# Performance work log

Measured on AMD Instinct MI355X. Metric: run time of the kernel, lower is better.

The kernel has to match this reference:

```python
import jax, jax.numpy as jnp
import numpy as np

B, S, HID = 1, 2048, 2048
NUM_HEADS, NUM_KV_HEADS, HEAD_DIM = 16, 4, 128
ROPE_THETA = 10000.0
EPS = 1e-6


def setup_inputs() -> dict:
    key = jax.random.key(0)
    ks = jax.random.split(key, 9)
    s = 0.02
    return {
        "hidden_states": jax.random.normal(ks[0], (B, S, HID), jnp.float32),
        "mu_prev": jax.random.normal(ks[1], (B, S, HID), jnp.float32),
        "wq": jax.random.normal(ks[2], (NUM_HEADS * HEAD_DIM, HID), jnp.float32) * s,
        "wk": jax.random.normal(ks[3], (NUM_KV_HEADS * HEAD_DIM, HID), jnp.float32) * s,
        "wv": jax.random.normal(ks[4], (NUM_KV_HEADS * HEAD_DIM, HID), jnp.float32) * s,
        "wo": jax.random.normal(ks[5], (HID, NUM_HEADS * HEAD_DIM), jnp.float32) * s,
        "wmq": jax.random.normal(ks[6], (NUM_HEADS * HEAD_DIM, HID), jnp.float32) * (s * 0.1),
        "wmk": jax.random.normal(ks[7], (NUM_KV_HEADS * HEAD_DIM, HID), jnp.float32) * (s * 0.1),
        "wmv": jax.random.normal(ks[8], (NUM_KV_HEADS * HEAD_DIM, HID), jnp.float32) * (s * 0.1),
        "q_norm_w": jnp.ones((HEAD_DIM,), jnp.float32),
        "k_norm_w": jnp.ones((HEAD_DIM,), jnp.float32),
    }


def _rmsnorm(x, w):
    var = jnp.mean(jnp.square(x), axis=-1, keepdims=True)
    return x * jax.lax.rsqrt(var + EPS) * w


def _rope_cos_sin(seq_len, dtype):
    inv_freq = 1.0 / (ROPE_THETA ** (jnp.arange(0, HEAD_DIM, 2, dtype=jnp.float32) / HEAD_DIM))
    freqs = jnp.arange(seq_len, dtype=jnp.float32)[:, None] * inv_freq[None, :]  # [S, D/2]
    emb = jnp.concatenate([freqs, freqs], axis=-1)  # [S, D]
    return jnp.cos(emb).astype(dtype), jnp.sin(emb).astype(dtype)


def _rotate_half(x):
    x1, x2 = jnp.split(x, 2, axis=-1)
    return jnp.concatenate([-x2, x1], axis=-1)


def reference(hidden_states, mu_prev, wq, wk, wv, wo, wmq, wmk, wmv, q_norm_w, k_norm_w):
    b, s, _ = hidden_states.shape
    # Fused mu-guided QKV projections (cat(x, mu) @ cat(W, Wm)^T == x@W^T + mu@Wm^T)
    q = hidden_states @ wq.T + mu_prev @ wmq.T  # [B,S,H*D]
    k = hidden_states @ wk.T + mu_prev @ wmk.T  # [B,S,KV*D]
    v = hidden_states @ wv.T + mu_prev @ wmv.T
    q = q.reshape(b, s, NUM_HEADS, HEAD_DIM).transpose(0, 2, 1, 3)      # [B,H,S,D]
    k = k.reshape(b, s, NUM_KV_HEADS, HEAD_DIM).transpose(0, 2, 1, 3)   # [B,KV,S,D]
    v = v.reshape(b, s, NUM_KV_HEADS, HEAD_DIM).transpose(0, 2, 1, 3)
    # per-head QK RMSNorm
    q = _rmsnorm(q, q_norm_w)
    k = _rmsnorm(k, k_norm_w)
    # RoPE
    cos, sin = _rope_cos_sin(s, q.dtype)
    q = q * cos + _rotate_half(q) * sin
    k = k * cos + _rotate_half(k) * sin
    # GQA attention without materializing repeated K/V: group query heads
    g = NUM_HEADS // NUM_KV_HEADS
    qg = q.reshape(b, NUM_KV_HEADS, g, s, HEAD_DIM)
    scale = 1.0 / jnp.sqrt(jnp.asarray(HEAD_DIM, q.dtype))
    scores = jnp.einsum('bkgqd,bkld->bkgql', qg, k) * scale  # [B,KV,G,S,S]
    causal = jnp.tril(jnp.ones((s, s), bool))
    scores = jnp.where(causal, scores, jnp.asarray(-jnp.inf, scores.dtype))
    probs = jax.nn.softmax(scores.astype(jnp.float32), axis=-1).astype(q.dtype)
    out = jnp.einsum('bkgql,bkld->bkgqd', probs, v)  # [B,KV,G,S,D]
    out = out.reshape(b, NUM_HEADS, s, HEAD_DIM).transpose(0, 2, 1, 3).reshape(b, s, NUM_HEADS * HEAD_DIM)
    return out @ wo.T
```

## Files before the change

kernel.cpp:

```cpp
#include <hip/hip_runtime.h>
#include <math.h>

#define SEQ 2048
#define HID_DIM 2048
#define NH 16
#define NKV 4
#define HD 128
#define QS 3072

typedef float  f4v  __attribute__((ext_vector_type(4)));
typedef __bf16 bf8v __attribute__((ext_vector_type(8)));
typedef __bf16 bf4v __attribute__((ext_vector_type(4)));
typedef __bf16 bf2v __attribute__((ext_vector_type(2)));

typedef __attribute__((address_space(1))) const void* gvp;
typedef __attribute__((address_space(3))) void*       svp;

__device__ __forceinline__ void gld16(const void* g, void* lds_wave_base) {
    __builtin_amdgcn_global_load_lds((gvp)g, (svp)lds_wave_base, 16, 0, 0);
}

__device__ __forceinline__ void wgb() {
    asm volatile("" ::: "memory");
    __builtin_amdgcn_s_barrier();
    asm volatile("" ::: "memory");
}
#define LGKM0 do { asm volatile("s_waitcnt lgkmcnt(0)" ::: "memory"); \
                   __builtin_amdgcn_sched_barrier(0); } while (0)
#define VMC(n) asm volatile("s_waitcnt vmcnt(" #n ")" ::: "memory")

__global__ __launch_bounds__(256)
void cvt_cat2(__bf16* __restrict__ dst, const float* __restrict__ s0,
              const float* __restrict__ s1, int rows, int kq)
{
    int i = blockIdx.x * 256 + threadIdx.x;
    if (i >= rows * kq * 2) return;
    int row = i / (2 * kq), c = i - row * 2 * kq;
    const float* s = (c < kq) ? s0 + ((size_t)row * kq + c) * 4
                              : s1 + ((size_t)row * kq + (c - kq)) * 4;
    float4 v = *reinterpret_cast<const float4*>(s);
    *reinterpret_cast<bf4v*>(dst + ((size_t)row * 2 * kq + c) * 4) =
        bf4v{ (__bf16)v.x, (__bf16)v.y, (__bf16)v.z, (__bf16)v.w };
}

__global__ __launch_bounds__(256)
void cvt(__bf16* __restrict__ dst, const float* __restrict__ src, int n4)
{
    int i = blockIdx.x * 256 + threadIdx.x;
    if (i >= n4) return;
    float4 v = *reinterpret_cast<const float4*>(src + (size_t)i * 4);
    *reinterpret_cast<bf4v*>(dst + (size_t)i * 4) =
        bf4v{ (__bf16)v.x, (__bf16)v.y, (__bf16)v.z, (__bf16)v.w };
}

__device__ __forceinline__ void stage_half(
    const __bf16* __restrict__ g, int ldk, int row0, int ktile, int half,
    char* buf, int w, int sr, int sc)
{
#pragma unroll
    for (int j = 0; j < 2; ++j) {
        int sid = w * 2 + j;
        int rb = half * 8 + (sid >> 1), cb = sid & 1;
        gld16(g + (size_t)(row0 + rb * 16 + sr) * ldk + ktile * 64 + cb * 32 + sc,
              buf + (rb * 2 + cb) * 1024);
    }
}

#define LOAD_A(BUF, MTB) \
    _Pragma("unroll") for (int mt = 0; mt < 4; ++mt) \
    _Pragma("unroll") for (int ks = 0; ks < 2; ++ks) \
        a[mt][ks] = *(const bf8v*)((BUF) + (((wm * 8 + (MTB) + mt) * 2 + ks) << 10) + frag_off);
#define LOAD_B(BUF, NTB, BR) \
    _Pragma("unroll") for (int nt = 0; nt < 2; ++nt) \
    _Pragma("unroll") for (int ks = 0; ks < 2; ++ks) \
        BR[nt][ks] = *(const bf8v*)((BUF) + (((wn * 4 + (NTB) + nt) * 2 + ks) << 10) + frag_off);
#define MFMA_Q(MTB, NTB, BR) \
    __builtin_amdgcn_s_setprio(1); \
    _Pragma("unroll") for (int mt = 0; mt < 4; ++mt) \
    _Pragma("unroll") for (int nt = 0; nt < 2; ++nt) \
    _Pragma("unroll") for (int ks = 0; ks < 2; ++ks) \
        acc[(MTB) + mt][(NTB) + nt] = __builtin_amdgcn_mfma_f32_16x16x32_bf16( \
            a[mt][ks], BR[nt][ks], acc[(MTB) + mt][(NTB) + nt], 0, 0, 0); \
    __builtin_amdgcn_s_setprio(0);

__global__ __launch_bounds__(512, 2)
void gemm_nt_8p(const __bf16* __restrict__ A, const __bf16* __restrict__ B,
                __bf16* __restrict__ P, int M, int N, int K, int KS)
{
    __shared__ __align__(1024) char lds[131072];
    char* A0 = lds;
    char* A1 = lds + 32768;
    char* B0 = lds + 65536;
    char* B1 = lds + 98304;

    const int tid = threadIdx.x, lane = tid & 63, w = tid >> 6;
    const int wm = w >> 2, wn = w & 3;
    const int mm = lane & 15, quad = lane >> 4;
    const int m0 = blockIdx.y * 256, n0 = blockIdx.x * 256;
    const int kt0 = (blockIdx.z * KS) >> 6;
    const int T = KS >> 6;

    const int g2 = lane ^ ((lane >> 4) & 3);
    const int sr = g2 >> 2, sc = (g2 & 3) * 8;
    const int gl = mm * 4 + quad;
    const int frag_off = (gl ^ ((gl >> 4) & 3)) << 4;

    f4v acc[8][4] = {};
    bf8v a[4][2], b01[2][2], b23[2][2];

    stage_half(A, K, m0, kt0,     0, A0, w, sr, sc);
    stage_half(A, K, m0, kt0,     1, A0, w, sr, sc);
    stage_half(B, K, n0, kt0,     0, B0, w, sr, sc);
    stage_half(B, K, n0, kt0,     1, B0, w, sr, sc);
    stage_half(A, K, m0, kt0 + 1, 0, A1, w, sr, sc);
    stage_half(A, K, m0, kt0 + 1, 1, A1, w, sr, sc);
    stage_half(B, K, n0, kt0 + 1, 0, B1, w, sr, sc);
    stage_half(B, K, n0, kt0 + 1, 1, B1, w, sr, sc);
    VMC(8);
    wgb();

    for (int t = 0; t < T; t += 2) {
        const bool more = (t + 2) < T;
        const int t2 = kt0 + t + 2, t3 = kt0 + t + 3;
        LOAD_A(A0, 0)
        LOAD_B(B0, 0, b01)
        wgb(); LGKM0;
        MFMA_Q(0, 0, b01)
        wgb();
        LOAD_B(B0, 2, b23)
        wgb(); LGKM0;
        MFMA_Q(0, 2, b23)
        wgb();
        LOAD_A(A0, 4)
        if (more) stage_half(B, K, n0, t2, 0, B0, w, sr, sc);
        wgb(); LGKM0;
        MFMA_Q(4, 2, b23)
        wgb();
        if (more) {
            stage_half(B, K, n0, t2, 1, B0, w, sr, sc);
            stage_half(A, K, m0, t2, 0, A0, w, sr, sc);
        }
        MFMA_Q(4, 0, b01)
        if (more) { VMC(6); } else { VMC(0); }
        wgb();
        LOAD_A(A1, 0)
        LOAD_B(B1, 0, b01)
        if (more) stage_half(A, K, m0, t2, 1, A0, w, sr, sc);
        wgb(); LGKM0;
        MFMA_Q(0, 0, b01)
        wgb();
        LOAD_B(B1, 2, b23)
        wgb(); LGKM0;
        MFMA_Q(0, 2, b23)
        wgb();
        LOAD_A(A1, 4)
        if (more) stage_half(B, K, n0, t3, 0, B1, w, sr, sc);
        wgb(); LGKM0;
        MFMA_Q(4, 2, b23)
        wgb();
        if (more) {
            stage_half(B, K, n0, t3, 1, B1, w, sr, sc);
            stage_half(A, K, m0, t3, 0, A1, w, sr, sc);
            stage_half(A, K, m0, t3, 1, A1, w, sr, sc);
        }
        MFMA_Q(4, 0, b01)
        if (more) { VMC(8); }
        wgb();
    }

    __bf16* Pz = P + (size_t)blockIdx.z * M * N;
#pragma unroll
    for (int mt = 0; mt < 8; ++mt)
#pragma unroll
        for (int nt = 0; nt < 4; ++nt)
#pragma unroll
            for (int r = 0; r < 4; ++r)
                Pz[(size_t)(m0 + wm * 128 + mt * 16 + quad * 4 + r) * N
                   + n0 + wn * 64 + nt * 16 + mm] = (__bf16)acc[mt][nt][r];
}

__global__ __launch_bounds__(256)
void add4(const __bf16* __restrict__ P, float* __restrict__ out, int n4)
{
    int i = blockIdx.x * 256 + threadIdx.x;
    if (i >= n4) return;
    float4 s = {0.f, 0.f, 0.f, 0.f};
#pragma unroll
    for (int z = 0; z < 4; ++z) {
        bf4v v = *reinterpret_cast<const bf4v*>(P + (size_t)z * n4 * 4 + (size_t)i * 4);
        s.x += (float)v[0]; s.y += (float)v[1]; s.z += (float)v[2]; s.w += (float)v[3];
    }
    *reinterpret_cast<float4*>(out + (size_t)i * 4) = s;
}

__global__ __launch_bounds__(64)
void norm_rope(__bf16* __restrict__ qkv ,
               const __bf16* __restrict__ p1,
               const float* __restrict__ qw, const float* __restrict__ kw)
{
    const int s = blockIdx.x, hh = blockIdx.y, l = threadIdx.x;
    const float* wn; float scale; int off;
    if (hh < NH) { off = hh * HD;               wn = qw; scale = 0.08838834764831845f; }
    else         { off = 2048 + (hh - NH) * HD; wn = kw; scale = 1.0f; }
    __bf16* p = qkv + (size_t)s * QS + off;
    const __bf16* q1 = p1 + (size_t)s * QS + off;
    float x0 = (float)p[l]      + (float)q1[l];
    float x1 = (float)p[l + 64] + (float)q1[l + 64];
    float ss = x0 * x0 + x1 * x1;
#pragma unroll
    for (int o = 32; o; o >>= 1) ss += __shfl_xor(ss, o);
    float inv = rsqrtf(ss * (1.0f / 128.0f) + 1e-6f);
    x0 *= inv * wn[l];
    x1 *= inv * wn[l + 64];
    float invf = exp2f(-(float)l * (13.287712379549449f / 64.0f));
    float ang  = (float)s * invf;
    float c, sn;
    sincosf(ang, &sn, &c);
    p[l]      = (__bf16)((x0 * c - x1 * sn) * scale);
    p[l + 64] = (__bf16)((x1 * c + x0 * sn) * scale);
}

__global__ __launch_bounds__(256)
void pack_k(const __bf16* __restrict__ qkv, __bf16* __restrict__ Kt)
{
    const int kt = blockIdx.x, kh = blockIdx.y, t = threadIdx.x;
    char* tile = (char*)Kt + ((size_t)(kh * 32 + kt)) * 16384;
    const __bf16* src = qkv + 2048 + kh * HD;
#pragma unroll
    for (int i = 0; i < 4; ++i) {
        int cid = t * 4 + i;
        int key = cid >> 4, pc = cid & 15;
        int c = pc ^ (key & 15);
        bf8v v = *reinterpret_cast<const bf8v*>(src + (size_t)(kt * 64 + key) * QS + c * 8);
        *reinterpret_cast<bf8v*>(tile + cid * 16) = v;
    }
}

__global__ __launch_bounds__(256)
void pack_v(const __bf16* __restrict__ qkv0, const __bf16* __restrict__ qkv1,
            __bf16* __restrict__ Vt)
{
    const int kt = blockIdx.x, kh = blockIdx.y, t = threadIdx.x;
    char* tile = (char*)Vt + ((size_t)(kh * 32 + kt)) * 16384;
    const __bf16* s0 = qkv0 + 2560 + kh * HD;
    const __bf16* s1 = qkv1 + 2560 + kh * HD;
#pragma unroll
    for (int i = 0; i < 4; ++i) {
        int cid = t * 4 + i;
        int d = cid >> 3, kcp = cid & 7;
        int kc = kcp ^ (d & 7);
        size_t base = (size_t)(kt * 64 + kc * 8) * QS + d;
        __bf16 tmp[8];
#pragma unroll
        for (int j = 0; j < 8; ++j)
            tmp[j] = (__bf16)((float)s0[base + (size_t)j * QS] +
                              (float)s1[base + (size_t)j * QS]);
        *reinterpret_cast<bf8v*>(tile + cid * 16) = *reinterpret_cast<bf8v*>(tmp);
    }
}

__global__ __launch_bounds__(256)
void attn_split(const __bf16* __restrict__ qkv,
                const __bf16* __restrict__ Kt, const __bf16* __restrict__ Vt,
                __bf16* __restrict__ Op, float* __restrict__ Lp)
{
    __shared__ char Ks[16384];
    __shared__ char Vs[16384];
    __shared__ char Ps[4][2048];

    const int c = blockIdx.x, qt = 31 - blockIdx.y, h = blockIdx.z;
    if (c * 8 > qt) return;
    const int kend = min(qt, c * 8 + 7);
    const int tid = threadIdx.x, lane = tid & 63, w = tid >> 6;
    const int mm = lane & 15, quad = lane >> 4;
    const int kh = h >> 2;

    bf8v aq[4];
    const __bf16* qbase = qkv + (size_t)(qt * 64 + w * 16 + mm) * QS + h * HD;
#pragma unroll
    for (int ks = 0; ks < 4; ++ks)
        aq[ks] = *reinterpret_cast<const bf8v*>(qbase + ks * 32 + quad * 8);

    float lp[4] = {};
    f4v oacc[8] = {};

    for (int kt = c * 8; kt <= kend; ++kt) {
        __syncthreads();
        const char* ktile = (const char*)Kt + ((size_t)(kh * 32 + kt)) * 16384;
        const char* vtile = (const char*)Vt + ((size_t)(kh * 32 + kt)) * 16384;
#pragma unroll
        for (int j = 0; j < 4; ++j) {
            int chunk = w * 4 + j;
            gld16(ktile + chunk * 1024 + lane * 16, Ks + chunk * 1024);
            gld16(vtile + chunk * 1024 + lane * 16, Vs + chunk * 1024);
        }
        __syncthreads();

        f4v s[4] = {};
#pragma unroll
        for (int ks = 0; ks < 4; ++ks)
#pragma unroll
            for (int c16 = 0; c16 < 4; ++c16) {
                bf8v b = *reinterpret_cast<const bf8v*>(
                    Ks + (c16 * 16 + mm) * 256 + (((ks * 4 + quad) ^ mm) << 4));
                s[c16] = __builtin_amdgcn_mfma_f32_16x16x32_bf16(aq[ks], b, s[c16], 0, 0, 0);
            }
        if (kt == qt) {
#pragma unroll
            for (int c16 = 0; c16 < 4; ++c16)
#pragma unroll
                for (int r = 0; r < 4; ++r)
                    if (c16 * 16 + mm > w * 16 + quad * 4 + r)
                        s[c16][r] = -__builtin_inff();
        }
        float pr[4][4];
#pragma unroll
        for (int c16 = 0; c16 < 4; ++c16)
#pragma unroll
            for (int r = 0; r < 4; ++r) {
                pr[c16][r] = __expf(s[c16][r]);
                lp[r] += pr[c16][r];
            }
#pragma unroll
        for (int c16 = 0; c16 < 4; ++c16)
#pragma unroll
            for (int r = 0; r < 4; ++r) {
                float mine  = pr[c16][r];
                float other = __shfl_xor(mine, 1);
                if ((mm & 1) == 0) {
                    int roww = quad * 4 + r;
                    int cc   = c16 * 2 + (mm >> 3);
                    *reinterpret_cast<bf2v*>(
                        &Ps[w][roww * 128 + ((cc ^ (roww & 7)) << 4) + (mm & 7) * 2]) =
                        bf2v{ (__bf16)mine, (__bf16)other };
                }
            }
        bf8v pa[2];
#pragma unroll
        for (int kb = 0; kb < 2; ++kb)
            pa[kb] = *reinterpret_cast<const bf8v*>(
                &Ps[w][mm * 128 + (((kb * 4 + quad) ^ (mm & 7)) << 4)]);
#pragma unroll
        for (int nb = 0; nb < 8; ++nb) {
            int d = nb * 16 + mm;
#pragma unroll
            for (int kb = 0; kb < 2; ++kb) {
                bf8v bv = *reinterpret_cast<const bf8v*>(
                    Vs + d * 128 + (((kb * 4 + quad) ^ (d & 7)) << 4));
                oacc[nb] = __builtin_amdgcn_mfma_f32_16x16x32_bf16(pa[kb], bv, oacc[nb], 0, 0, 0);
            }
        }
    }
#pragma unroll
    for (int off = 1; off < 16; off <<= 1)
#pragma unroll
        for (int r = 0; r < 4; ++r) lp[r] += __shfl_xor(lp[r], off);
#pragma unroll
    for (int r = 0; r < 4; ++r) {
        int row = qt * 64 + w * 16 + quad * 4 + r;
        size_t obase = ((size_t)(c * 16 + h) * SEQ + row) * HD;
#pragma unroll
        for (int nb = 0; nb < 8; ++nb)
            Op[obase + nb * 16 + mm] = (__bf16)oacc[nb][r];
        if (mm == 0)
            Lp[(size_t)(c * 16 + h) * SEQ + row] = lp[r];
    }
}

__global__ __launch_bounds__(64)
void combine(const __bf16* __restrict__ Op, const float* __restrict__ Lp,
             __bf16* __restrict__ ab)
{
    const int row = blockIdx.x, h = blockIdx.y, l = threadIdx.x;
    const int nch = (row >> 9) + 1;
    float L = 0.f, a0 = 0.f, a1 = 0.f;
    for (int c = 0; c < nch; ++c) {
        L += Lp[(size_t)(c * 16 + h) * SEQ + row];
        bf2v p = *reinterpret_cast<const bf2v*>(
            Op + ((size_t)(c * 16 + h) * SEQ + row) * HD + 2 * l);
        a0 += (float)p[0];
        a1 += (float)p[1];
    }
    float inv = 1.f / L;
    *reinterpret_cast<bf2v*>(ab + (size_t)row * (NH * HD) + h * HD + 2 * l) =
        bf2v{ (__bf16)(a0 * inv), (__bf16)(a1 * inv) };
}

extern "C" void kernel_launch(void* const* d_in, const int* in_sizes, int n_in,
                              void* d_out, int out_size, void* d_ws, size_t ws_size,
                              hipStream_t stream)
{
    const float* hs  = (const float*)d_in[0];
    const float* mu  = (const float*)d_in[1];
    const float* wq  = (const float*)d_in[2];
    const float* wk  = (const float*)d_in[3];
    const float* wv  = (const float*)d_in[4];
    const float* wo  = (const float*)d_in[5];
    const float* wmq = (const float*)d_in[6];
    const float* wmk = (const float*)d_in[7];
    const float* wmv = (const float*)d_in[8];
    const float* qw  = (const float*)d_in[9];
    const float* kw  = (const float*)d_in[10];
    float* out = (float*)d_out;

    char* ws = (char*)d_ws;
    __bf16* Wcat = (__bf16*)(ws + 0);
    __bf16* Acat = (__bf16*)(ws + 25165824);
    __bf16* Wo   = (__bf16*)(ws + 41943040);
    __bf16* qkvp = (__bf16*)(ws + 50331648);
    __bf16* ab   = (__bf16*)(ws + 75497472);
    __bf16* Ktl  = (__bf16*)(ws + 0);
    __bf16* Vtl  = (__bf16*)(ws + 2097152);
    __bf16* Opart= (__bf16*)(ws + 4194304);
    float*  Lpart= (float*) (ws + 37748736);
    __bf16* outp = (__bf16*)(ws + 0);

    cvt_cat2<<<dim3((2048 * 1024 + 255) / 256), 256, 0, stream>>>(Acat, hs, mu, 2048, 512);
    cvt_cat2<<<dim3((2048 * 1024 + 255) / 256), 256, 0, stream>>>(Wcat, wq, wmq, 2048, 512);
    cvt_cat2<<<dim3((512 * 1024 + 255) / 256), 256, 0, stream>>>(Wcat + (size_t)2048 * 4096, wk, wmk, 512, 512);
    cvt_cat2<<<dim3((512 * 1024 + 255) / 256), 256, 0, stream>>>(Wcat + (size_t)2560 * 4096, wv, wmv, 512, 512);
    cvt<<<dim3((1024 * 1024 + 255) / 256), 256, 0, stream>>>(Wo, wo, 1024 * 1024);

    gemm_nt_8p<<<dim3(QS / 256, SEQ / 256, 2), 512, 0, stream>>>(Acat, Wcat, qkvp, SEQ, QS, 2 * HID_DIM, HID_DIM);
    norm_rope<<<dim3(SEQ, NH + NKV), dim3(64), 0, stream>>>(qkvp, qkvp + (size_t)SEQ * QS, qw, kw);
    pack_k<<<dim3(32, NKV), 256, 0, stream>>>(qkvp, Ktl);
    pack_v<<<dim3(32, NKV), 256, 0, stream>>>(qkvp, qkvp + (size_t)SEQ * QS, Vtl);
    attn_split<<<dim3(4, 32, NH), 256, 0, stream>>>(qkvp, Ktl, Vtl, Opart, Lpart);
    combine<<<dim3(SEQ, NH), 64, 0, stream>>>(Opart, Lpart, ab);
    gemm_nt_8p<<<dim3(HID_DIM / 256, SEQ / 256, 4), 512, 0, stream>>>(ab, Wo, outp, SEQ, HID_DIM, NH * HD, 512);
    add4<<<dim3((1024 * 1024 + 255) / 256), 256, 0, stream>>>(outp, out, 1024 * 1024);
}
```

Baseline: 359.7 us.

## Software-pipeline LDS fragment loads across MFMA quadrants in GEMM kernel

Restructures the GEMM main loop so the LDS fragment reads for the next quadrant are issued before the current quadrant's MFMAs. Explicit lgkmcnt waits are removed, and A and B register fragments are double-buffered (aLo/aHi, b01e/b01o). The LDS XOR swizzle is dropped in favour of a plain linear fragment layout. Global staging is regrouped into whole-tile loads with a full vmcnt(0) wait, and a peeled epilogue handles the last two k-tiles. The aim is to overlap LDS latency with MFMA work, at the cost of more registers, possible LDS bank conflicts without the swizzle, and stricter global-load waits.

```diff
diff --git a/kernel.cpp b/kernel.cpp
--- a/kernel.cpp
+++ b/kernel.cpp
@@ -25,8 +25,6 @@
     __builtin_amdgcn_s_barrier();
     asm volatile("" ::: "memory");
 }
-#define LGKM0 do { asm volatile("s_waitcnt lgkmcnt(0)" ::: "memory"); \
-                   __builtin_amdgcn_sched_barrier(0); } while (0)
 #define VMC(n) asm volatile("s_waitcnt vmcnt(" #n ")" ::: "memory")
 
 __global__ __launch_bounds__(256)
@@ -65,26 +63,33 @@
               buf + (rb * 2 + cb) * 1024);
     }
 }
-
-#define LOAD_A(BUF, MTB) \
+__device__ __forceinline__ void stage_tile(
+    const __bf16* __restrict__ g, int ldk, int row0, int ktile,
+    char* buf, int w, int sr, int sc)
+{
+    stage_half(g, ldk, row0, ktile, 0, buf, w, sr, sc);
+    stage_half(g, ldk, row0, ktile, 1, buf, w, sr, sc);
+}
+
+#define LOAD_AF(DST, BUF, MTB) \
     _Pragma("unroll") for (int mt = 0; mt < 4; ++mt) \
     _Pragma("unroll") for (int ks = 0; ks < 2; ++ks) \
-        a[mt][ks] = *(const bf8v*)((BUF) + (((wm * 8 + (MTB) + mt) * 2 + ks) << 10) + frag_off);
-#define LOAD_B(BUF, NTB, BR) \
+        DST[mt][ks] = *(const bf8v*)((BUF) + (((wm * 8 + (MTB) + mt) * 2 + ks) << 10) + frag_off);
+#define LOAD_BF(DST, BUF, NTB) \
     _Pragma("unroll") for (int nt = 0; nt < 2; ++nt) \
     _Pragma("unroll") for (int ks = 0; ks < 2; ++ks) \
-        BR[nt][ks] = *(const bf8v*)((BUF) + (((wn * 4 + (NTB) + nt) * 2 + ks) << 10) + frag_off);
-#define MFMA_Q(MTB, NTB, BR) \
+        DST[nt][ks] = *(const bf8v*)((BUF) + (((wn * 4 + (NTB) + nt) * 2 + ks) << 10) + frag_off);
+#define MFMA_Q(MTB, NTB, AR, BR) \
     __builtin_amdgcn_s_setprio(1); \
     _Pragma("unroll") for (int mt = 0; mt < 4; ++mt) \
     _Pragma("unroll") for (int nt = 0; nt < 2; ++nt) \
     _Pragma("unroll") for (int ks = 0; ks < 2; ++ks) \
         acc[(MTB) + mt][(NTB) + nt] = __builtin_amdgcn_mfma_f32_16x16x32_bf16( \
-            a[mt][ks], BR[nt][ks], acc[(MTB) + mt][(NTB) + nt], 0, 0, 0); \
+            AR[mt][ks], BR[nt][ks], acc[(MTB) + mt][(NTB) + nt], 0, 0, 0); \
     __builtin_amdgcn_s_setprio(0);
 
 __global__ __launch_bounds__(512, 2)
-void gemm_nt_8p(const __bf16* __restrict__ A, const __bf16* __restrict__ B,
+void gemm_nt_pl(const __bf16* __restrict__ A, const __bf16* __restrict__ B,
                 __bf16* __restrict__ P, int M, int N, int K, int KS)
 {
     __shared__ __align__(1024) char lds[131072];
@@ -100,73 +105,76 @@
     const int kt0 = (blockIdx.z * KS) >> 6;
     const int T = KS >> 6;
 
-    const int g2 = lane ^ ((lane >> 4) & 3);
-    const int sr = g2 >> 2, sc = (g2 & 3) * 8;
-    const int gl = mm * 4 + quad;
-    const int frag_off = (gl ^ ((gl >> 4) & 3)) << 4;
+    const int sr = lane >> 2, sc = (lane & 3) * 8;
+    const int frag_off = (mm * 4 + quad) << 4;
 
     f4v acc[8][4] = {};
-    bf8v a[4][2], b01[2][2], b23[2][2];
-
-    stage_half(A, K, m0, kt0,     0, A0, w, sr, sc);
-    stage_half(A, K, m0, kt0,     1, A0, w, sr, sc);
-    stage_half(B, K, n0, kt0,     0, B0, w, sr, sc);
-    stage_half(B, K, n0, kt0,     1, B0, w, sr, sc);
-    stage_half(A, K, m0, kt0 + 1, 0, A1, w, sr, sc);
-    stage_half(A, K, m0, kt0 + 1, 1, A1, w, sr, sc);
-    stage_half(B, K, n0, kt0 + 1, 0, B1, w, sr, sc);
-    stage_half(B, K, n0, kt0 + 1, 1, B1, w, sr, sc);
+    bf8v aLo[4][2], aHi[4][2], b01e[2][2], b01o[2][2], b23[2][2];
+
+    stage_tile(A, K, m0, kt0,     A0, w, sr, sc);
+    stage_tile(B, K, n0, kt0,     B0, w, sr, sc);
+    stage_tile(A, K, m0, kt0 + 1, A1, w, sr, sc);
+    stage_tile(B, K, n0, kt0 + 1, B1, w, sr, sc);
     VMC(8);
     wgb();
-
-    for (int t = 0; t < T; t += 2) {
-        const bool more = (t + 2) < T;
-        const int t2 = kt0 + t + 2, t3 = kt0 + t + 3;
-        LOAD_A(A0, 0)
-        LOAD_B(B0, 0, b01)
-        wgb(); LGKM0;
-        MFMA_Q(0, 0, b01)
-        wgb();
-        LOAD_B(B0, 2, b23)
-        wgb(); LGKM0;
-        MFMA_Q(0, 2, b23)
-        wgb();
-        LOAD_A(A0, 4)
-        if (more) stage_half(B, K, n0, t2, 0, B0, w, sr, sc);
-        wgb(); LGKM0;
-        MFMA_Q(4, 2, b23)
-        wgb();
-        if (more) {
-            stage_half(B, K, n0, t2, 1, B0, w, sr, sc);
-            stage_half(A, K, m0, t2, 0, A0, w, sr, sc);
-        }
-        MFMA_Q(4, 0, b01)
-        if (more) { VMC(6); } else { VMC(0); }
-        wgb();
-        LOAD_A(A1, 0)
-        LOAD_B(B1, 0, b01)
-        if (more) stage_half(A, K, m0, t2, 1, A0, w, sr, sc);
-        wgb(); LGKM0;
-        MFMA_Q(0, 0, b01)
-        wgb();
-        LOAD_B(B1, 2, b23)
-        wgb(); LGKM0;
-        MFMA_Q(0, 2, b23)
-        wgb();
-        LOAD_A(A1, 4)
-        if (more) stage_half(B, K, n0, t3, 0, B1, w, sr, sc);
-        wgb(); LGKM0;
-        MFMA_Q(4, 2, b23)
-        wgb();
-        if (more) {
-            stage_half(B, K, n0, t3, 1, B1, w, sr, sc);
-            stage_half(A, K, m0, t3, 0, A1, w, sr, sc);
-            stage_half(A, K, m0, t3, 1, A1, w, sr, sc);
-        }
-        MFMA_Q(4, 0, b01)
-        if (more) { VMC(8); }
-        wgb();
-    }
+    LOAD_AF(aLo, A0, 0)
+    LOAD_BF(b01e, B0, 0)
+
+    const int nbody = (T - 2) >> 1;
+    for (int it = 0; it < nbody; ++it) {
+        const int t2 = kt0 + 2 * it + 2, t3 = t2 + 1;
+        LOAD_BF(b23, B0, 2)
+        MFMA_Q(0, 0, aLo, b01e)
+        wgb();
+        LOAD_AF(aHi, A0, 4)
+        MFMA_Q(0, 2, aLo, b23)
+        VMC(0);
+        wgb();
+        LOAD_AF(aLo, A1, 0)
+        stage_tile(B, K, n0, t2, B0, w, sr, sc);
+        MFMA_Q(4, 2, aHi, b23)
+        wgb();
+        LOAD_BF(b01o, B1, 0)
+        stage_tile(A, K, m0, t2, A0, w, sr, sc);
+        MFMA_Q(4, 0, aHi, b01e)
+        wgb();
+        LOAD_BF(b23, B1, 2)
+        MFMA_Q(0, 0, aLo, b01o)
+        wgb();
+        LOAD_AF(aHi, A1, 4)
+        MFMA_Q(0, 2, aLo, b23)
+        VMC(0);
+        wgb();
+        LOAD_AF(aLo, A0, 0)
+        stage_tile(B, K, n0, t3, B1, w, sr, sc);
+        MFMA_Q(4, 2, aHi, b23)
+        wgb();
+        LOAD_BF(b01e, B0, 0)
+        stage_tile(A, K, m0, t3, A1, w, sr, sc);
+        MFMA_Q(4, 0, aHi, b01o)
+        wgb();
+    }
+    LOAD_BF(b23, B0, 2)
+    MFMA_Q(0, 0, aLo, b01e)
+    wgb();
+    LOAD_AF(aHi, A0, 4)
+    MFMA_Q(0, 2, aLo, b23)
+    VMC(0);
+    wgb();
+    LOAD_AF(aLo, A1, 0)
+    MFMA_Q(4, 2, aHi, b23)
+    wgb();
+    LOAD_BF(b01o, B1, 0)
+    MFMA_Q(4, 0, aHi, b01e)
+    wgb();
+    LOAD_BF(b23, B1, 2)
+    MFMA_Q(0, 0, aLo, b01o)
+    wgb();
+    LOAD_AF(aHi, A1, 4)
+    MFMA_Q(0, 2, aLo, b23)
+    wgb();
+    MFMA_Q(4, 2, aHi, b23)
+    MFMA_Q(4, 0, aHi, b01o)
 
     __bf16* Pz = P + (size_t)blockIdx.z * M * N;
 #pragma unroll
@@ -421,12 +429,12 @@
     cvt_cat2<<<dim3((512 * 1024 + 255) / 256), 256, 0, stream>>>(Wcat + (size_t)2560 * 4096, wv, wmv, 512, 512);
     cvt<<<dim3((1024 * 1024 + 255) / 256), 256, 0, stream>>>(Wo, wo, 1024 * 1024);
 
-    gemm_nt_8p<<<dim3(QS / 256, SEQ / 256, 2), 512, 0, stream>>>(Acat, Wcat, qkvp, SEQ, QS, 2 * HID_DIM, HID_DIM);
+    gemm_nt_pl<<<dim3(QS / 256, SEQ / 256, 2), 512, 0, stream>>>(Acat, Wcat, qkvp, SEQ, QS, 2 * HID_DIM, HID_DIM);
     norm_rope<<<dim3(SEQ, NH + NKV), dim3(64), 0, stream>>>(qkvp, qkvp + (size_t)SEQ * QS, qw, kw);
     pack_k<<<dim3(32, NKV), 256, 0, stream>>>(qkvp, Ktl);
     pack_v<<<dim3(32, NKV), 256, 0, stream>>>(qkvp, qkvp + (size_t)SEQ * QS, Vtl);
     attn_split<<<dim3(4, 32, NH), 256, 0, stream>>>(qkvp, Ktl, Vtl, Opart, Lpart);
     combine<<<dim3(SEQ, NH), 64, 0, stream>>>(Opart, Lpart, ab);
-    gemm_nt_8p<<<dim3(HID_DIM / 256, SEQ / 256, 4), 512, 0, stream>>>(ab, Wo, outp, SEQ, HID_DIM, NH * HD, 512);
+    gemm_nt_pl<<<dim3(HID_DIM / 256, SEQ / 256, 4), 512, 0, stream>>>(ab, Wo, outp, SEQ, HID_DIM, NH * HD, 512);
     add4<<<dim3((1024 * 1024 + 255) / 256), 256, 0, stream>>>(outp, out, 1024 * 1024);
 }
```

Result: no change. 355.2 us (-1.3%).
